# Optimization experiments

Hardware: AMD Instinct MI355X
Metric: run time of the kernel (lower is better)

The kernel has to match this reference:

```python
import jax, jax.numpy as jnp
import numpy as np

N_POINTS_TOTAL = 1_000_000
FEAT_DIM = 64
B = 128            # number of point clouds (segments)
LATENT_DIM = 512
NUM_POINTS = 2048  # decoder output points per cloud
EPS = 1e-5


def setup_inputs() -> dict:
    key = jax.random.key(0)
    ks = jax.random.split(key, 12)
    s = 0.02
    feat = jax.random.normal(ks[0], (N_POINTS_TOTAL, FEAT_DIM), dtype=jnp.float32)
    # sorted segment ids in [0, B); with 1M points and 128 segments every segment is nonempty
    batch = jnp.sort(jax.random.randint(ks[1], (N_POINTS_TOTAL,), 0, B, dtype=jnp.int64))
    return {
        "feat": feat,
        "batch": batch,
        "ln_g": jnp.ones((FEAT_DIM,), jnp.float32),
        "ln_b": jnp.zeros((FEAT_DIM,), jnp.float32),
        # Linear weights stored [in, out] (transposed vs torch)
        "proj_w": jax.random.normal(ks[2], (FEAT_DIM, LATENT_DIM), jnp.float32) * s,
        "proj_b": jnp.zeros((LATENT_DIM,), jnp.float32),
        "w1": jax.random.normal(ks[3], (LATENT_DIM, 256), jnp.float32) * s,
        "b1": jnp.zeros((256,), jnp.float32),
        "w2": jax.random.normal(ks[4], (256, 512), jnp.float32) * s,
        "b2": jnp.zeros((512,), jnp.float32),
        "w3": jax.random.normal(ks[5], (512, NUM_POINTS * 3), jnp.float32) * s,
        "b3": jnp.zeros((NUM_POINTS * 3,), jnp.float32),
    }


def reference(feat, batch, ln_g, ln_b, proj_w, proj_b, w1, b1, w2, b2, w3, b3):
    # Ragged per-cloud max pool: replaces the per-sample Python loop with one segment-max.
    pooled = jax.ops.segment_max(feat, batch, num_segments=B)  # [B, 64]
    # LayerNorm(64)
    mu = jnp.mean(pooled, axis=-1, keepdims=True)
    var = jnp.mean(jnp.square(pooled - mu), axis=-1, keepdims=True)
    x = (pooled - mu) * jax.lax.rsqrt(var + EPS) * ln_g + ln_b
    # proj + decoder MLP
    latent = x @ proj_w + proj_b                               # [B, 512]
    h = jax.nn.relu(latent @ w1 + b1)                          # [B, 256]
    h = jax.nn.relu(h @ w2 + b2)                               # [B, 512]
    out = h @ w3 + b3                                          # [B, NUM_POINTS*3]
    return out.reshape(-1, NUM_POINTS, 3)
```

## Files before the change

### kernel.cpp

```cpp
#include <hip/hip_runtime.h>
#include <hip/hip_bf16.h>

#define N_POINTS 1000000
#define FEAT 64
#define BSEG 128
#define EPS 1e-5f
#define CHUNK 1024
#define NBLK_SEG ((N_POINTS + CHUNK - 1) / CHUNK)

__device__ __forceinline__ unsigned ordered_enc(float f) {
    unsigned u = __float_as_uint(f);
    return (u & 0x80000000u) ? ~u : (u | 0x80000000u);
}
__device__ __forceinline__ float ordered_dec(unsigned v) {
    unsigned u = (v & 0x80000000u) ? (v & 0x7fffffffu) : ~v;
    return __uint_as_float(u);
}

#define ENC_NEG_INF 0x007FFFFFu

__global__ void k_init(unsigned* __restrict__ pool) {
    int i = blockIdx.x * blockDim.x + threadIdx.x;
    if (i < BSEG * FEAT) pool[i] = ENC_NEG_INF;
}

__global__ __launch_bounds__(256) void k_segmax(const float4* __restrict__ feat,
                                                const int* __restrict__ batch,
                                                unsigned* __restrict__ pool) {
    __shared__ unsigned short sb[CHUNK];
    __shared__ unsigned spool[4 * FEAT];
    const int t = threadIdx.x;
    const int base = blockIdx.x * CHUNK;
    int rem = N_POINTS - base;
    if (rem > CHUNK) rem = CHUNK;

    for (int i = t; i < CHUNK; i += 256)
        sb[i] = (i < rem) ? (unsigned short)batch[base + i] : (unsigned short)0xFFFF;
    spool[t] = 0u;
    __syncthreads();

    const int seg0 = sb[0];
    const int q = t & 7;
    const int r = t >> 3;

    float4 m0 = make_float4(-INFINITY, -INFINITY, -INFINITY, -INFINITY);
    float4 m1 = m0;
    int cur = -1;

    auto flush = [&](int seg, float4 a, float4 b) {
        unsigned e[8] = { ordered_enc(a.x), ordered_enc(a.y), ordered_enc(a.z), ordered_enc(a.w),
                          ordered_enc(b.x), ordered_enc(b.y), ordered_enc(b.z), ordered_enc(b.w) };
        int slot = seg - seg0;
        if (slot >= 0 && slot < 4) {
            unsigned* p = &spool[slot * FEAT + q * 8];
            #pragma unroll
            for (int j = 0; j < 8; ++j) atomicMax(&p[j], e[j]);
        } else {
            unsigned* p = &pool[seg * FEAT + q * 8];
            #pragma unroll
            for (int j = 0; j < 8; ++j) atomicMax(&p[j], e[j]);
        }
    };

    for (int i = r; i < rem; i += 32) {
        const float4* p = &feat[(size_t)(base + i) * 16 + q * 2];
        float4 v0 = p[0];
        float4 v1 = p[1];
        int seg = sb[i];
        if (seg != cur) {
            if (cur >= 0) flush(cur, m0, m1);
            cur = seg;
            m0 = make_float4(-INFINITY, -INFINITY, -INFINITY, -INFINITY);
            m1 = m0;
        }
        m0.x = fmaxf(m0.x, v0.x); m0.y = fmaxf(m0.y, v0.y);
        m0.z = fmaxf(m0.z, v0.z); m0.w = fmaxf(m0.w, v0.w);
        m1.x = fmaxf(m1.x, v1.x); m1.y = fmaxf(m1.y, v1.y);
        m1.z = fmaxf(m1.z, v1.z); m1.w = fmaxf(m1.w, v1.w);
    }
    if (cur >= 0) flush(cur, m0, m1);
    __syncthreads();

    unsigned v = spool[t];
    if (v != 0u) {
        int slot = t >> 6;
        atomicMax(&pool[(seg0 + slot) * FEAT + (t & 63)], v);
    }
}

__global__ __launch_bounds__(256) void k_mlp(const unsigned* __restrict__ pool,
                                             const float* __restrict__ ln_g,
                                             const float* __restrict__ ln_b,
                                             const float* __restrict__ pw,
                                             const float* __restrict__ pb,
                                             const float* __restrict__ w1,
                                             const float* __restrict__ b1,
                                             const float* __restrict__ w2,
                                             const float* __restrict__ b2,
                                             float* __restrict__ h2out) {
    __shared__ float xn[64];
    __shared__ float lat[512];
    __shared__ float h1s[256];
    const int b = blockIdx.x, t = threadIdx.x;

    if (t < 64) {
        float x = ordered_dec(pool[b * 64 + t]);
        float s = x;
        #pragma unroll
        for (int off = 32; off > 0; off >>= 1) s += __shfl_xor(s, off, 64);
        float mu = s * (1.0f / 64.0f);
        float d = x - mu;
        float s2 = d * d;
        #pragma unroll
        for (int off = 32; off > 0; off >>= 1) s2 += __shfl_xor(s2, off, 64);
        float var = s2 * (1.0f / 64.0f);
        xn[t] = d * rsqrtf(var + EPS) * ln_g[t] + ln_b[t];
    }
    __syncthreads();

    {
        float a0 = pb[t], a1 = pb[t + 256];
        #pragma unroll 8
        for (int j = 0; j < 64; ++j) {
            float xj = xn[j];
            a0 = fmaf(xj, pw[j * 512 + t], a0);
            a1 = fmaf(xj, pw[j * 512 + t + 256], a1);
        }
        lat[t] = a0; lat[t + 256] = a1;
    }
    __syncthreads();

    {
        float a = b1[t];
        #pragma unroll 8
        for (int j = 0; j < 512; ++j)
            a = fmaf(lat[j], w1[j * 256 + t], a);
        h1s[t] = fmaxf(a, 0.0f);
    }
    __syncthreads();

    {
        float a0 = b2[t], a1 = b2[t + 256];
        #pragma unroll 8
        for (int j = 0; j < 256; ++j) {
            float hj = h1s[j];
            a0 = fmaf(hj, w2[j * 512 + t], a0);
            a1 = fmaf(hj, w2[j * 512 + t + 256], a1);
        }
        h2out[b * 512 + t] = fmaxf(a0, 0.0f);
        h2out[b * 512 + t + 256] = fmaxf(a1, 0.0f);
    }
}

#define RS 136
__global__ __launch_bounds__(512) void k_final(const float* __restrict__ h2,
                                               const float* __restrict__ w3,
                                               const float* __restrict__ b3,
                                               float* __restrict__ out) {
    __shared__ float h2s[128 * RS];
    const int t = threadIdx.x;
    const int tx = t & 15;
    const int ty = t >> 4;
    const int c = blockIdx.x * 64 + tx * 4;
    const int r0 = ty * 4;

    float4 bias = *(const float4*)&b3[c];
    float4 acc[4] = {bias, bias, bias, bias};

    const float4* h2g = (const float4*)h2;
    for (int kc = 0; kc < 512; kc += 128) {
        __syncthreads();
        #pragma unroll
        for (int it = 0; it < 8; ++it) {
            int idx = it * 512 + t;
            int rr = idx >> 5;
            int kq = idx & 31;
            float4 v = h2g[rr * 128 + (kc >> 2) + kq];
            *(float4*)&h2s[rr * RS + kq * 4] = v;
        }
        __syncthreads();
        #pragma unroll 4
        for (int k = 0; k < 128; ++k) {
            float4 w = *(const float4*)&w3[(size_t)(kc + k) * 6144 + c];
            float a0 = h2s[(r0 + 0) * RS + k];
            float a1 = h2s[(r0 + 1) * RS + k];
            float a2 = h2s[(r0 + 2) * RS + k];
            float a3 = h2s[(r0 + 3) * RS + k];
            acc[0].x = fmaf(a0, w.x, acc[0].x); acc[0].y = fmaf(a0, w.y, acc[0].y);
            acc[0].z = fmaf(a0, w.z, acc[0].z); acc[0].w = fmaf(a0, w.w, acc[0].w);
            acc[1].x = fmaf(a1, w.x, acc[1].x); acc[1].y = fmaf(a1, w.y, acc[1].y);
            acc[1].z = fmaf(a1, w.z, acc[1].z); acc[1].w = fmaf(a1, w.w, acc[1].w);
            acc[2].x = fmaf(a2, w.x, acc[2].x); acc[2].y = fmaf(a2, w.y, acc[2].y);
            acc[2].z = fmaf(a2, w.z, acc[2].z); acc[2].w = fmaf(a2, w.w, acc[2].w);
            acc[3].x = fmaf(a3, w.x, acc[3].x); acc[3].y = fmaf(a3, w.y, acc[3].y);
            acc[3].z = fmaf(a3, w.z, acc[3].z); acc[3].w = fmaf(a3, w.w, acc[3].w);
        }
    }
    #pragma unroll
    for (int i = 0; i < 4; ++i)
        *(float4*)&out[(size_t)(r0 + i) * 6144 + c] = acc[i];
}

extern "C" void kernel_launch(void* const* d_in, const int* in_sizes, int n_in,
                              void* d_out, int out_size, void* d_ws, size_t ws_size,
                              hipStream_t stream) {
    const float* feat  = (const float*)d_in[0];
    const int*   batch = (const int*)d_in[1];
    const float* ln_g  = (const float*)d_in[2];
    const float* ln_b  = (const float*)d_in[3];
    const float* pw    = (const float*)d_in[4];
    const float* pb    = (const float*)d_in[5];
    const float* w1    = (const float*)d_in[6];
    const float* b1    = (const float*)d_in[7];
    const float* w2    = (const float*)d_in[8];
    const float* b2    = (const float*)d_in[9];
    const float* w3    = (const float*)d_in[10];
    const float* b3    = (const float*)d_in[11];
    float* out = (float*)d_out;

    unsigned* pool = (unsigned*)d_ws;
    float* h2buf = (float*)d_ws + BSEG * FEAT;

    k_init<<<(BSEG * FEAT + 255) / 256, 256, 0, stream>>>(pool);
    k_segmax<<<NBLK_SEG, 256, 0, stream>>>((const float4*)feat, batch, pool);
    k_mlp<<<BSEG, 256, 0, stream>>>(pool, ln_g, ln_b, pw, pb, w1, b1, w2, b2, h2buf);
    k_final<<<96, 512, 0, stream>>>(h2buf, w3, b3, out);
}
```

Measured before the change: 503.1 us.

## Split-K MLP over 1024 threads, memset-based pool init, vectorized LDS reads

The MLP kernel now runs 1024 threads per cloud. Each layer's reduction dimension is split across thread groups, and the partial sums are combined through shared memory, which shortens the serial dot-product chains. The ordered-float encoding is shifted by a bias so that the -inf sentinel encodes as zero; this lets a memset replace the init kernel launch. The final GEMM reads four activations per float4 LDS load instead of scalar loads. The trade-offs are extra barriers and shared-memory traffic in the MLP.

```diff
diff --git a/kernel.cpp b/kernel.cpp
--- a/kernel.cpp
+++ b/kernel.cpp
@@ -8,20 +8,17 @@
 #define CHUNK 1024
 #define NBLK_SEG ((N_POINTS + CHUNK - 1) / CHUNK)
 
+#define ENC_BIAS 0x007FFFFFu
+
 __device__ __forceinline__ unsigned ordered_enc(float f) {
     unsigned u = __float_as_uint(f);
-    return (u & 0x80000000u) ? ~u : (u | 0x80000000u);
+    unsigned o = (u & 0x80000000u) ? ~u : (u | 0x80000000u);
+    return o - ENC_BIAS;
 }
 __device__ __forceinline__ float ordered_dec(unsigned v) {
-    unsigned u = (v & 0x80000000u) ? (v & 0x7fffffffu) : ~v;
+    unsigned o = v + ENC_BIAS;
+    unsigned u = (o & 0x80000000u) ? (o & 0x7fffffffu) : ~o;
     return __uint_as_float(u);
-}
-
-#define ENC_NEG_INF 0x007FFFFFu
-
-__global__ void k_init(unsigned* __restrict__ pool) {
-    int i = blockIdx.x * blockDim.x + threadIdx.x;
-    if (i < BSEG * FEAT) pool[i] = ENC_NEG_INF;
 }
 
 __global__ __launch_bounds__(256) void k_segmax(const float4* __restrict__ feat,
@@ -88,19 +85,20 @@
     }
 }
 
-__global__ __launch_bounds__(256) void k_mlp(const unsigned* __restrict__ pool,
-                                             const float* __restrict__ ln_g,
-                                             const float* __restrict__ ln_b,
-                                             const float* __restrict__ pw,
-                                             const float* __restrict__ pb,
-                                             const float* __restrict__ w1,
-                                             const float* __restrict__ b1,
-                                             const float* __restrict__ w2,
-                                             const float* __restrict__ b2,
-                                             float* __restrict__ h2out) {
+__global__ __launch_bounds__(1024) void k_mlp(const unsigned* __restrict__ pool,
+                                              const float* __restrict__ ln_g,
+                                              const float* __restrict__ ln_b,
+                                              const float* __restrict__ pw,
+                                              const float* __restrict__ pb,
+                                              const float* __restrict__ w1,
+                                              const float* __restrict__ b1,
+                                              const float* __restrict__ w2,
+                                              const float* __restrict__ b2,
+                                              float* __restrict__ h2out) {
     __shared__ float xn[64];
     __shared__ float lat[512];
     __shared__ float h1s[256];
+    __shared__ float red[1024];
     const int b = blockIdx.x, t = threadIdx.x;
 
     if (t < 64) {
@@ -119,37 +117,47 @@
     __syncthreads();
 
     {
-        float a0 = pb[t], a1 = pb[t + 256];
+        int o = t & 511, h = t >> 9;
+        float a = 0.0f;
+        #pragma unroll
+        for (int j = 0; j < 32; ++j) {
+            int k = h * 32 + j;
+            a = fmaf(xn[k], pw[k * 512 + o], a);
+        }
+        red[t] = a;
+    }
+    __syncthreads();
+    if (t < 512) lat[t] = red[t] + red[t + 512] + pb[t];
+    __syncthreads();
+
+    {
+        int o = t & 255, h = t >> 8;
+        float a = 0.0f;
         #pragma unroll 8
-        for (int j = 0; j < 64; ++j) {
-            float xj = xn[j];
-            a0 = fmaf(xj, pw[j * 512 + t], a0);
-            a1 = fmaf(xj, pw[j * 512 + t + 256], a1);
-        }
-        lat[t] = a0; lat[t + 256] = a1;
-    }
+        for (int j = 0; j < 128; ++j) {
+            int k = h * 128 + j;
+            a = fmaf(lat[k], w1[k * 256 + o], a);
+        }
+        red[t] = a;
+    }
+    __syncthreads();
+    if (t < 256)
+        h1s[t] = fmaxf(red[t] + red[t + 256] + red[t + 512] + red[t + 768] + b1[t], 0.0f);
     __syncthreads();
 
     {
-        float a = b1[t];
+        int o = t & 511, h = t >> 9;
+        float a = 0.0f;
         #pragma unroll 8
-        for (int j = 0; j < 512; ++j)
-            a = fmaf(lat[j], w1[j * 256 + t], a);
-        h1s[t] = fmaxf(a, 0.0f);
-    }
-    __syncthreads();
-
-    {
-        float a0 = b2[t], a1 = b2[t + 256];
-        #pragma unroll 8
-        for (int j = 0; j < 256; ++j) {
-            float hj = h1s[j];
-            a0 = fmaf(hj, w2[j * 512 + t], a0);
-            a1 = fmaf(hj, w2[j * 512 + t + 256], a1);
-        }
-        h2out[b * 512 + t] = fmaxf(a0, 0.0f);
-        h2out[b * 512 + t + 256] = fmaxf(a1, 0.0f);
-    }
+        for (int j = 0; j < 128; ++j) {
+            int k = h * 128 + j;
+            a = fmaf(h1s[k], w2[k * 512 + o], a);
+        }
+        red[t] = a;
+    }
+    __syncthreads();
+    if (t < 512)
+        h2out[b * 512 + t] = fmaxf(red[t] + red[t + 512] + b2[t], 0.0f);
 }
 
 #define RS 136
@@ -179,21 +187,27 @@
             *(float4*)&h2s[rr * RS + kq * 4] = v;
         }
         __syncthreads();
-        #pragma unroll 4
-        for (int k = 0; k < 128; ++k) {
-            float4 w = *(const float4*)&w3[(size_t)(kc + k) * 6144 + c];
-            float a0 = h2s[(r0 + 0) * RS + k];
-            float a1 = h2s[(r0 + 1) * RS + k];
-            float a2 = h2s[(r0 + 2) * RS + k];
-            float a3 = h2s[(r0 + 3) * RS + k];
-            acc[0].x = fmaf(a0, w.x, acc[0].x); acc[0].y = fmaf(a0, w.y, acc[0].y);
-            acc[0].z = fmaf(a0, w.z, acc[0].z); acc[0].w = fmaf(a0, w.w, acc[0].w);
-            acc[1].x = fmaf(a1, w.x, acc[1].x); acc[1].y = fmaf(a1, w.y, acc[1].y);
-            acc[1].z = fmaf(a1, w.z, acc[1].z); acc[1].w = fmaf(a1, w.w, acc[1].w);
-            acc[2].x = fmaf(a2, w.x, acc[2].x); acc[2].y = fmaf(a2, w.y, acc[2].y);
-            acc[2].z = fmaf(a2, w.z, acc[2].z); acc[2].w = fmaf(a2, w.w, acc[2].w);
-            acc[3].x = fmaf(a3, w.x, acc[3].x); acc[3].y = fmaf(a3, w.y, acc[3].y);
-            acc[3].z = fmaf(a3, w.z, acc[3].z); acc[3].w = fmaf(a3, w.w, acc[3].w);
+        for (int k = 0; k < 128; k += 4) {
+            float4 A0 = *(const float4*)&h2s[(r0 + 0) * RS + k];
+            float4 A1 = *(const float4*)&h2s[(r0 + 1) * RS + k];
+            float4 A2 = *(const float4*)&h2s[(r0 + 2) * RS + k];
+            float4 A3 = *(const float4*)&h2s[(r0 + 3) * RS + k];
+            #pragma unroll
+            for (int kk = 0; kk < 4; ++kk) {
+                float4 w = *(const float4*)&w3[(size_t)(kc + k + kk) * 6144 + c];
+                float a0 = (kk == 0) ? A0.x : (kk == 1) ? A0.y : (kk == 2) ? A0.z : A0.w;
+                float a1 = (kk == 0) ? A1.x : (kk == 1) ? A1.y : (kk == 2) ? A1.z : A1.w;
+                float a2 = (kk == 0) ? A2.x : (kk == 1) ? A2.y : (kk == 2) ? A2.z : A2.w;
+                float a3 = (kk == 0) ? A3.x : (kk == 1) ? A3.y : (kk == 2) ? A3.z : A3.w;
+                acc[0].x = fmaf(a0, w.x, acc[0].x); acc[0].y = fmaf(a0, w.y, acc[0].y);
+                acc[0].z = fmaf(a0, w.z, acc[0].z); acc[0].w = fmaf(a0, w.w, acc[0].w);
+                acc[1].x = fmaf(a1, w.x, acc[1].x); acc[1].y = fmaf(a1, w.y, acc[1].y);
+                acc[1].z = fmaf(a1, w.z, acc[1].z); acc[1].w = fmaf(a1, w.w, acc[1].w);
+                acc[2].x = fmaf(a2, w.x, acc[2].x); acc[2].y = fmaf(a2, w.y, acc[2].y);
+                acc[2].z = fmaf(a2, w.z, acc[2].z); acc[2].w = fmaf(a2, w.w, acc[2].w);
+                acc[3].x = fmaf(a3, w.x, acc[3].x); acc[3].y = fmaf(a3, w.y, acc[3].y);
+                acc[3].z = fmaf(a3, w.z, acc[3].z); acc[3].w = fmaf(a3, w.w, acc[3].w);
+            }
         }
     }
     #pragma unroll
@@ -221,8 +235,8 @@
     unsigned* pool = (unsigned*)d_ws;
     float* h2buf = (float*)d_ws + BSEG * FEAT;
 
-    k_init<<<(BSEG * FEAT + 255) / 256, 256, 0, stream>>>(pool);
+    hipMemsetAsync(pool, 0, BSEG * FEAT * sizeof(unsigned), stream);
     k_segmax<<<NBLK_SEG, 256, 0, stream>>>((const float4*)feat, batch, pool);
-    k_mlp<<<BSEG, 256, 0, stream>>>(pool, ln_g, ln_b, pw, pb, w1, b1, w2, b2, h2buf);
+    k_mlp<<<BSEG, 1024, 0, stream>>>(pool, ln_g, ln_b, pw, pb, w1, b1, w2, b2, h2buf);
     k_final<<<96, 512, 0, stream>>>(h2buf, w3, b3, out);
 }
```

Result: faster. 472.6 us (-6.1%).
